# Kernel optimization log

Hardware: AMD Instinct MI355X
Metric: run time of the kernel (lower is better)

Reference implementation:

```python
import jax, jax.numpy as jnp
import numpy as np

N, E, P = 50000, 800000, 100000
IN, HID, H, L = 128, 128, 8, 3
D = HID // H


def setup_inputs() -> dict:
    key = jax.random.key(0)
    ks = jax.random.split(key, 24)
    rn = lambda k, shape, s: (jax.random.normal(k, shape, jnp.float32) * s)
    inp = {
        'x': jax.random.normal(ks[0], (N, IN), jnp.float32),
        'edge_src': jax.random.randint(ks[1], (E,), 0, N, jnp.int32),
        'edge_dst': jax.random.randint(ks[2], (E,), 0, N, jnp.int32),
        'edge_w': jax.random.uniform(ks[3], (E,), jnp.float32),
        'pos_src': jax.random.randint(ks[4], (P,), 0, N, jnp.int32),
        'pos_dst': jax.random.randint(ks[5], (P,), 0, N, jnp.int32),
        'neg_src': jax.random.randint(ks[6], (P,), 0, N, jnp.int32),
        'neg_dst': jax.random.randint(ks[7], (P,), 0, N, jnp.int32),
        # input projection
        'W_in': rn(ks[8], (IN, HID), IN ** -0.5),
        'b_in': jnp.zeros((HID,), jnp.float32),
        # per-layer HGT params (single ntype/etype -> plain matrices)
        'Wk': rn(ks[9], (L, HID, HID), HID ** -0.5),
        'Wq': rn(ks[10], (L, HID, HID), HID ** -0.5),
        'Wv': rn(ks[11], (L, HID, HID), HID ** -0.5),
        'att_w': rn(ks[12], (L, H, D, D), D ** -0.5),
        'msg_w': rn(ks[13], (L, H, D, D), D ** -0.5),
        'pri': jnp.ones((L, H), jnp.float32),
        'Wa': rn(ks[14], (L, HID, HID), HID ** -0.5),
        'skip': jnp.ones((L,), jnp.float32),
        # predictor MLP
        'W1': rn(ks[15], (HID, HID // 2), HID ** -0.5),
        'b1': jnp.zeros((HID // 2,), jnp.float32),
        'W2': rn(ks[16], (HID // 2, HID // 4), (HID // 2) ** -0.5),
        'b2': jnp.zeros((HID // 4,), jnp.float32),
        'W3': rn(ks[17], (HID // 4, 1), (HID // 4) ** -0.5),
        'b3': jnp.zeros((1,), jnp.float32),
    }
    return inp


def _hgt_forward(x, edge_src, edge_dst, edge_w, pos_src, pos_dst, neg_src, neg_dst,
                 W_in, b_in, Wk, Wq, Wv, att_w, msg_w, pri, Wa, skip,
                 W1, b1, W2, b2, W3, b3):
    n = x.shape[0]
    nheads = att_w.shape[1]
    d = att_w.shape[2]
    sqrt_d = jnp.asarray(d ** 0.5, x.dtype)
    h = jax.nn.relu(x @ W_in + b_in)
    nlayers = Wk.shape[0]
    for l in range(nlayers):
        k = (h @ Wk[l]).reshape(n, nheads, d)
        q = (h @ Wq[l]).reshape(n, nheads, d)
        v = (h @ Wv[l]).reshape(n, nheads, d)
        # relation-specific per-head transforms (etype constant -> node-level)
        kw = jnp.einsum('nhd,hde->nhe', k, att_w[l])
        mv = jnp.einsum('nhd,hde->nhe', v, msg_w[l])
        # per-edge attention logits [E, H]
        a = (kw[edge_src] * q[edge_dst]).sum(-1) * pri[l] / sqrt_d
        # edge softmax grouped by destination node
        amax = jax.ops.segment_max(a, edge_dst, num_segments=n)[edge_dst]
        ex = jnp.exp(a - amax)
        denom = jax.ops.segment_sum(ex, edge_dst, num_segments=n)[edge_dst]
        attn = ex / denom
        # weighted messages + scatter-sum  [E,H,D] -> [N,H,D]
        m = mv[edge_src] * edge_w[:, None, None] * attn[:, :, None]
        agg = jax.ops.segment_sum(m, edge_dst, num_segments=n).reshape(n, nheads * d)
        hn = agg @ Wa[l]  # linear_a (dropout is identity in eval)
        alpha = jax.nn.sigmoid(skip[l])
        h = hn * alpha + h * (1.0 - alpha)
        if l != nlayers - 1:
            h = jax.nn.relu(h)  # inter-layer relu (dropout identity)
    def predictor(z):
        z = jax.nn.leaky_relu(z @ W1 + b1, 0.2)
        z = jax.nn.leaky_relu(z @ W2 + b2, 0.2)
        return z @ W3 + b3
    h_pos = predictor(h[pos_src] * h[pos_dst])
    h_neg = predictor(h[neg_src] * h[neg_dst])
    return h_pos, h_neg, h


def reference(x, edge_src, edge_dst, edge_w, pos_src, pos_dst, neg_src, neg_dst,
              W_in, b_in, Wk, Wq, Wv, att_w, msg_w, pri, Wa, skip,
              W1, b1, W2, b2, W3, b3):
    return _hgt_forward(x, edge_src, edge_dst, edge_w, pos_src, pos_dst,
                        neg_src, neg_dst, W_in, b_in, Wk, Wq, Wv, att_w,
                        msg_w, pri, Wa, skip, W1, b1, W2, b2, W3, b3)
```

## Files before the change

### kernel.cpp

```cpp
#include <hip/hip_runtime.h>
#include <cstddef>

#define N_NODES 50000
#define N_EDGES 800000
#define N_PAIRS 100000

typedef float floatx4 __attribute__((ext_vector_type(4)));
typedef _Float16 half2v __attribute__((ext_vector_type(2)));
typedef _Float16 half4v __attribute__((ext_vector_type(4)));
typedef _Float16 half8v __attribute__((ext_vector_type(8)));

__device__ inline size_t packA(int m, int k, int K) {
  return ((size_t)((m >> 4) * (K >> 5) + (k >> 5)) << 9) +
         ((((unsigned)k >> 3) & 3) << 7) + ((m & 15) << 3) + (k & 7);
}

__device__ inline float fold_val(int l, int r, int j, const float* Wk, const float* Wq,
                                 const float* Wv, const float* att, const float* msg,
                                 const float* pri) {
  if (j >= 128 && j < 256) return Wq[(l * 128 + r) * 128 + (j - 128)];
  int jj = j & 127, hh = jj >> 4, e = jj & 15;
  const float* W = (j < 128) ? Wk : Wv;
  const float* T = (j < 128) ? att : msg;
  float s = 0.f;
#pragma unroll
  for (int d = 0; d < 16; d++)
    s += W[(l * 128 + r) * 128 + hh * 16 + d] * T[((l * 8 + hh) * 16 + d) * 16 + e];
  if (j < 128) s *= pri[l * 8 + hh] * 0.25f;
  return s;
}

__global__ void wprep_kernel(const float* __restrict__ W_in, const float* __restrict__ Wk,
                             const float* __restrict__ Wq, const float* __restrict__ Wv,
                             const float* __restrict__ att, const float* __restrict__ msg,
                             const float* __restrict__ pri, const float* __restrict__ Wa,
                             const float* __restrict__ W1, const float* __restrict__ W2,
                             _Float16* Wint, _Float16* Wcat, _Float16* Waf,
                             _Float16* W1f, _Float16* W2f) {
  int gid = blockIdx.x * 256 + threadIdx.x;
  float v;
  _Float16* dt;
  size_t o;
  if (gid < 16384) {
    int n = gid >> 7, k = gid & 127;
    v = W_in[k * 128 + n];
    dt = Wint; o = packA(n, k, 128);
  } else if (gid < 163840) {
    int t = gid - 16384;
    int l = t / 49152, u = t - l * 49152;
    int n = u >> 7, k = u & 127;
    v = fold_val(l, k, n, Wk, Wq, Wv, att, msg, pri);
    dt = Wcat + (size_t)l * 49152;
    o = packA(n, k, 128);
  } else if (gid < 212992) {
    int t = gid - 163840;
    int l = t / 16384, u = t & 16383;
    int n = u >> 7, k = u & 127;
    v = Wa[(size_t)l * 16384 + k * 128 + n];
    dt = Waf + (size_t)l * 16384;
    o = packA(n, k, 128);
  } else if (gid < 221184) {
    int u = gid - 212992;
    int n = u >> 7, k = u & 127;
    v = W1[k * 64 + n];
    dt = W1f; o = packA(n, k, 128);
  } else if (gid < 225280) {
    int u = gid - 221184;
    int n = u >> 6, k = u & 63;
    v = (n < 32) ? W2[k * 32 + n] : 0.f;
    dt = W2f; o = packA(n, k, 64);
  } else {
    return;
  }
  dt[o] = (_Float16)v;
}

__global__ void hist_kernel(const int* __restrict__ dst, int* __restrict__ deg, int E) {
  int g = blockIdx.x * blockDim.x + threadIdx.x;
  if (g < E) atomicAdd(&deg[dst[g]], 1);
}

__global__ void scanA_kernel(const int* __restrict__ deg, int* __restrict__ offs,
                             int* __restrict__ bsum, int n) {
  __shared__ int sm[256];
  int t = threadIdx.x;
  int i = blockIdx.x * 256 + t;
  int v = (i < n) ? ((deg[i] + 7) & ~7) : 0;
  sm[t] = v;
  __syncthreads();
  for (int off = 1; off < 256; off <<= 1) {
    int u = (t >= off) ? sm[t - off] : 0;
    __syncthreads();
    sm[t] += u;
    __syncthreads();
  }
  if (i < n) offs[i] = sm[t] - v;
  if (t == 255) bsum[blockIdx.x] = sm[255];
}

__global__ void scanB_kernel(const int* __restrict__ bsum, int* __restrict__ boff,
                             int* __restrict__ offs, int nb, int n) {
  __shared__ int sm[256];
  int t = threadIdx.x;
  int v = (t < nb) ? bsum[t] : 0;
  sm[t] = v;
  __syncthreads();
  for (int off = 1; off < 256; off <<= 1) {
    int u = (t >= off) ? sm[t - off] : 0;
    __syncthreads();
    sm[t] += u;
    __syncthreads();
  }
  boff[t] = sm[t] - v;
  if (t == nb - 1) offs[n] = sm[t];
}

__global__ void scanC_kernel(int* __restrict__ offs, const int* __restrict__ boff,
                             int* __restrict__ cursor, int n) {
  int i = blockIdx.x * 256 + threadIdx.x;
  if (i < n) {
    int o = offs[i] + boff[blockIdx.x];
    offs[i] = o;
    cursor[i] = o;
  }
}

__global__ void scatter_kernel(const int* __restrict__ src, const int* __restrict__ dst,
                               const float* __restrict__ w, int* __restrict__ cursor,
                               int2* __restrict__ eld, int E) {
  int g = blockIdx.x * blockDim.x + threadIdx.x;
  if (g < E) {
    int d = dst[g];
    int p = atomicAdd(&cursor[d], 1);
    eld[p] = make_int2(src[g], __float_as_int(w[g]));
  }
}

__global__ void bhist_kernel(const int* __restrict__ deg, int* __restrict__ bh, int n) {
  __shared__ int lh[256];
  int t = threadIdx.x;
  lh[t] = 0;
  __syncthreads();
  int i = blockIdx.x * 256 + t;
  if (i < n) atomicAdd(&lh[min(deg[i], 255)], 1);
  __syncthreads();
  if (lh[t]) atomicAdd(&bh[t], lh[t]);
}
__global__ void bscan_kernel(const int* __restrict__ bh, int* __restrict__ bcur) {
  __shared__ int sm[256];
  int t = threadIdx.x;
  int v = bh[255 - t];
  sm[t] = v;
  __syncthreads();
  for (int off = 1; off < 256; off <<= 1) {
    int u = (t >= off) ? sm[t - off] : 0;
    __syncthreads();
    sm[t] += u;
    __syncthreads();
  }
  bcur[255 - t] = sm[t] - v;
}
__global__ void bscatter_kernel(const int* __restrict__ deg, int* __restrict__ bcur,
                                int* __restrict__ perm, int n) {
  __shared__ int lh[256], lbase[256];
  int t = threadIdx.x;
  lh[t] = 0;
  __syncthreads();
  int i = blockIdx.x * 256 + t;
  int b = 0, local = 0;
  if (i < n) {
    b = min(deg[i], 255);
    local = atomicAdd(&lh[b], 1);
  }
  __syncthreads();
  int cnt = lh[t];
  lbase[t] = cnt ? atomicAdd(&bcur[t], cnt) : 0;
  __syncthreads();
  if (i < n) perm[lbase[b] + local] = i;
}

template <int FIRST>
__global__ __launch_bounds__(256) void fused_layer(
    const float* __restrict__ x, const _Float16* __restrict__ aggp,
    const _Float16* __restrict__ Wg1, const float* __restrict__ bias,
    const float* __restrict__ skipv, _Float16* __restrict__ hbuf,
    const _Float16* __restrict__ Wcat_l,
    _Float16* __restrict__ kwmv, _Float16* __restrict__ qbuf, int M) {
  int tid = threadIdx.x;
  int wave = tid >> 6, lane = tid & 63;
  int l16 = lane & 15, q = lane >> 4;
  int g = q, mloc = l16;
  int tile = blockIdx.x * 4 + wave;
  int m0 = tile * 16;
  bool alive = m0 < M;
  int tileC = alive ? tile : 0;

  __shared__ _Float16 htile_s[4][2048];
  __shared__ float ldsT_s[4][16 * 68];
  _Float16* htile = htile_s[wave];
  float* myT = ldsT_s[wave];

  half8v a[4];
#pragma unroll
  for (int kc = 0; kc < 4; kc++) {
    if (FIRST) {
      int row = min(m0 + l16, M - 1);
      const float* p = x + (size_t)row * 128 + kc * 32 + q * 8;
      float4 u0 = *(const float4*)p, u1 = *(const float4*)(p + 4);
      float f[8] = {u0.x, u0.y, u0.z, u0.w, u1.x, u1.y, u1.z, u1.w};
      half8v hv;
#pragma unroll
      for (int i = 0; i < 8; i++) hv[i] = (_Float16)f[i];
      a[kc] = hv;
    } else {
      a[kc] = *(const half8v*)(aggp + (size_t)tileC * 2048 + (kc << 9) + lane * 8);
    }
  }

  float alpha = 1.f, beta = 0.f;
  if (!FIRST) {
    float sv = *skipv;
    alpha = 1.f / (1.f + __expf(-sv));
    beta = 1.f - alpha;
  }

  floatx4 acc1[8];
#pragma unroll
  for (int nt = 0; nt < 8; nt++) acc1[nt] = (floatx4){0.f, 0.f, 0.f, 0.f};
#pragma unroll
  for (int kc = 0; kc < 4; kc++) {
    half8v b[8];
#pragma unroll
    for (int nt = 0; nt < 8; nt++)
      b[nt] = *(const half8v*)(Wg1 + (size_t)nt * 2048 + (kc << 9) + lane * 8);
#pragma unroll
    for (int nt = 0; nt < 8; nt++)
      acc1[nt] = __builtin_amdgcn_mfma_f32_16x16x32_f16(a[kc], b[nt], acc1[nt], 0, 0, 0);
  }

#pragma unroll
  for (int p = 0; p < 2; p++) {
    __syncthreads();
#pragma unroll
    for (int ntl = 0; ntl < 4; ntl++)
#pragma unroll
      for (int r = 0; r < 4; r++)
        myT[(q * 4 + r) * 68 + ntl * 16 + l16] = acc1[p * 4 + ntl][r];
    __syncthreads();
#pragma unroll
    for (int kc2 = 0; kc2 < 2; kc2++) {
      const float* rp = myT + mloc * 68 + kc2 * 32 + g * 8;
      floatx4 v0 = *(const floatx4*)rp;
      floatx4 v1 = *(const floatx4*)(rp + 4);
      float vals[8] = {v0[0], v0[1], v0[2], v0[3], v1[0], v1[1], v1[2], v1[3]};
      int col0 = p * 64 + kc2 * 32 + g * 8;
      size_t pbaseL = ((size_t)(tileC * 4 + (col0 >> 5)) << 9) + (size_t)lane * 8;
      if (FIRST) {
        float4 bb0 = *(const float4*)&bias[col0];
        float4 bb1 = *(const float4*)&bias[col0 + 4];
        float bbv[8] = {bb0.x, bb0.y, bb0.z, bb0.w, bb1.x, bb1.y, bb1.z, bb1.w};
#pragma unroll
        for (int j = 0; j < 8; j++) vals[j] = fmaxf(vals[j] + bbv[j], 0.f);
      } else {
        half8v hv = *(const half8v*)(hbuf + pbaseL);
#pragma unroll
        for (int j = 0; j < 8; j++)
          vals[j] = fmaxf(alpha * vals[j] + beta * (float)hv[j], 0.f);
      }
      half8v h8;
#pragma unroll
      for (int j = 0; j < 8; j++) h8[j] = (_Float16)vals[j];
      *(half8v*)(htile + (((p * 2 + kc2) << 9) + (g << 7) + (mloc << 3))) = h8;
      if (alive) *(half8v*)(hbuf + pbaseL) = h8;
    }
  }

  for (int c = 0; c < 6; c++) {
    floatx4 acc2[4];
#pragma unroll
    for (int nt = 0; nt < 4; nt++) acc2[nt] = (floatx4){0.f, 0.f, 0.f, 0.f};
#pragma unroll
    for (int kc = 0; kc < 4; kc++) {
      half8v af = *(const half8v*)(htile + ((kc << 9) + lane * 8));
      half8v b[4];
#pragma unroll
      for (int nt = 0; nt < 4; nt++)
        b[nt] = *(const half8v*)(Wcat_l + (size_t)(c * 4 + nt) * 2048 + (kc << 9) + lane * 8);
#pragma unroll
      for (int nt = 0; nt < 4; nt++)
        acc2[nt] = __builtin_amdgcn_mfma_f32_16x16x32_f16(af, b[nt], acc2[nt], 0, 0, 0);
    }
    __syncthreads();
#pragma unroll
    for (int ntl = 0; ntl < 4; ntl++)
#pragma unroll
      for (int r = 0; r < 4; r++)
        myT[(q * 4 + r) * 68 + ntl * 16 + l16] = acc2[ntl][r];
    __syncthreads();
    if (alive) {
      int row = m0 + mloc;
#pragma unroll
      for (int kc2 = 0; kc2 < 2; kc2++) {
        const float* rp = myT + mloc * 68 + kc2 * 32 + g * 8;
        floatx4 v0 = *(const floatx4*)rp;
        floatx4 v1 = *(const floatx4*)(rp + 4);
        int col0 = c * 64 + kc2 * 32 + g * 8;
        int region = col0 >> 7;
        if (region == 1) {
          half8v h8;
#pragma unroll
          for (int j = 0; j < 4; j++) {
            h8[j] = (_Float16)v0[j];
            h8[j + 4] = (_Float16)v1[j];
          }
          *(half8v*)&qbuf[(size_t)row * 128 + (col0 - 128)] = h8;
        } else {
          int cc = col0 & 127;
          size_t base = (size_t)row * 256 + (size_t)(cc >> 2) * 8 + (region == 2 ? 4 : 0);
          half4v h0, h1;
#pragma unroll
          for (int j = 0; j < 4; j++) {
            h0[j] = (_Float16)v0[j];
            h1[j] = (_Float16)v1[j];
          }
          *(half4v*)&kwmv[base] = h0;
          *(half4v*)&kwmv[base + 8] = h1;
        }
      }
    }
  }
}

__global__ __launch_bounds__(256) void gemm_last(
    const _Float16* __restrict__ aggp, const _Float16* __restrict__ Wg1,
    const float* __restrict__ skipv, const _Float16* __restrict__ hbuf,
    float* __restrict__ hfinal, _Float16* __restrict__ hrow, int M) {
  int tid = threadIdx.x;
  int wave = tid >> 6, lane = tid & 63;
  int l16 = lane & 15, q = lane >> 4;
  int g = q, mloc = l16;
  int tile = blockIdx.x * 4 + wave;
  int m0 = tile * 16;
  bool alive = m0 < M;
  int tileC = alive ? tile : 0;

  __shared__ float ldsT_s[4][16 * 68];
  float* myT = ldsT_s[wave];

  half8v a[4];
#pragma unroll
  for (int kc = 0; kc < 4; kc++)
    a[kc] = *(const half8v*)(aggp + (size_t)tileC * 2048 + (kc << 9) + lane * 8);

  float sv = *skipv;
  float alpha = 1.f / (1.f + __expf(-sv));
  float beta = 1.f - alpha;

  floatx4 acc1[8];
#pragma unroll
  for (int nt = 0; nt < 8; nt++) acc1[nt] = (floatx4){0.f, 0.f, 0.f, 0.f};
#pragma unroll
  for (int kc = 0; kc < 4; kc++) {
    half8v b[8];
#pragma unroll
    for (int nt = 0; nt < 8; nt++)
      b[nt] = *(const half8v*)(Wg1 + (size_t)nt * 2048 + (kc << 9) + lane * 8);
#pragma unroll
    for (int nt = 0; nt < 8; nt++)
      acc1[nt] = __builtin_amdgcn_mfma_f32_16x16x32_f16(a[kc], b[nt], acc1[nt], 0, 0, 0);
  }

#pragma unroll
  for (int p = 0; p < 2; p++) {
    __syncthreads();
#pragma unroll
    for (int ntl = 0; ntl < 4; ntl++)
#pragma unroll
      for (int r = 0; r < 4; r++)
        myT[(q * 4 + r) * 68 + ntl * 16 + l16] = acc1[p * 4 + ntl][r];
    __syncthreads();
    if (alive) {
      int row = m0 + mloc;
#pragma unroll
      for (int kc2 = 0; kc2 < 2; kc2++) {
        const float* rp = myT + mloc * 68 + kc2 * 32 + g * 8;
        floatx4 v0 = *(const floatx4*)rp;
        floatx4 v1 = *(const floatx4*)(rp + 4);
        float vals[8] = {v0[0], v0[1], v0[2], v0[3], v1[0], v1[1], v1[2], v1[3]};
        int col0 = p * 64 + kc2 * 32 + g * 8;
        size_t pbase = ((size_t)(tile * 4 + (col0 >> 5)) << 9) + (size_t)lane * 8;
        half8v hv = *(const half8v*)(hbuf + pbase);
#pragma unroll
        for (int j = 0; j < 8; j++) vals[j] = alpha * vals[j] + beta * (float)hv[j];
        *(float4*)&hfinal[(size_t)row * 128 + col0] =
            make_float4(vals[0], vals[1], vals[2], vals[3]);
        *(float4*)&hfinal[(size_t)row * 128 + col0 + 4] =
            make_float4(vals[4], vals[5], vals[6], vals[7]);
        half8v h8;
#pragma unroll
        for (int j = 0; j < 8; j++) h8[j] = (_Float16)vals[j];
        *(half8v*)&hrow[(size_t)row * 128 + col0] = h8;
      }
    }
  }
}

__global__ __launch_bounds__(256) void pred_fused(
    const _Float16* __restrict__ hrow,
    const int* __restrict__ ps, const int* __restrict__ pd,
    const int* __restrict__ ns, const int* __restrict__ nd,
    const _Float16* __restrict__ W1f, const float* __restrict__ b1,
    const _Float16* __restrict__ W2f, const float* __restrict__ b2,
    const float* __restrict__ W3, const float* __restrict__ b3,
    float* __restrict__ outd, int M) {
  int tid = threadIdx.x;
  int wave = tid >> 6, lane = tid & 63;
  int l16 = lane & 15, q = lane >> 4;
  int g = q, mloc = l16;
  int tile = blockIdx.x * 4 + wave;
  int m0 = tile * 16;
  bool alive = m0 < M;

  __shared__ _Float16 t1_s[4][1024];
  __shared__ float ldsT_s[4][16 * 68];
  _Float16* t1tile = t1_s[wave];
  float* myT = ldsT_s[wave];

  int gr = min(m0 + l16, M - 1);
  bool pos = gr < N_PAIRS;
  int idx = pos ? gr : gr - N_PAIRS;
  int pa = pos ? ps[idx] : ns[idx];
  int pb = pos ? pd[idx] : nd[idx];

  half8v a[4];
#pragma unroll
  for (int kc = 0; kc < 4; kc++) {
    int kbase = kc * 32 + q * 8;
    half8v ha = *(const half8v*)(hrow + (size_t)pa * 128 + kbase);
    half8v hb = *(const half8v*)(hrow + (size_t)pb * 128 + kbase);
    a[kc] = ha * hb;
  }

  floatx4 acc1[4];
#pragma unroll
  for (int nt = 0; nt < 4; nt++) acc1[nt] = (floatx4){0.f, 0.f, 0.f, 0.f};
#pragma unroll
  for (int kc = 0; kc < 4; kc++) {
    half8v b[4];
#pragma unroll
    for (int nt = 0; nt < 4; nt++)
      b[nt] = *(const half8v*)(W1f + (size_t)nt * 2048 + (kc << 9) + lane * 8);
#pragma unroll
    for (int nt = 0; nt < 4; nt++)
      acc1[nt] = __builtin_amdgcn_mfma_f32_16x16x32_f16(a[kc], b[nt], acc1[nt], 0, 0, 0);
  }

  __syncthreads();
#pragma unroll
  for (int ntl = 0; ntl < 4; ntl++)
#pragma unroll
    for (int r = 0; r < 4; r++)
      myT[(q * 4 + r) * 68 + ntl * 16 + l16] = acc1[ntl][r];
  __syncthreads();
#pragma unroll
  for (int kc2 = 0; kc2 < 2; kc2++) {
    const float* rp = myT + mloc * 68 + kc2 * 32 + g * 8;
    floatx4 v0 = *(const floatx4*)rp;
    floatx4 v1 = *(const floatx4*)(rp + 4);
    float vals[8] = {v0[0], v0[1], v0[2], v0[3], v1[0], v1[1], v1[2], v1[3]};
    int col0 = kc2 * 32 + g * 8;
    float4 bb0 = *(const float4*)&b1[col0];
    float4 bb1 = *(const float4*)&b1[col0 + 4];
    float bbv[8] = {bb0.x, bb0.y, bb0.z, bb0.w, bb1.x, bb1.y, bb1.z, bb1.w};
    half8v h8;
#pragma unroll
    for (int j = 0; j < 8; j++) {
      float v = vals[j] + bbv[j];
      v = v > 0.f ? v : 0.2f * v;
      h8[j] = (_Float16)v;
    }
    *(half8v*)(t1tile + ((kc2 << 9) + (g << 7) + (mloc << 3))) = h8;
  }

  floatx4 acc2[2];
#pragma unroll
  for (int nt = 0; nt < 2; nt++) acc2[nt] = (floatx4){0.f, 0.f, 0.f, 0.f};
#pragma unroll
  for (int kc = 0; kc < 2; kc++) {
    half8v af = *(const half8v*)(t1tile + ((kc << 9) + lane * 8));
    half8v b[2];
#pragma unroll
    for (int nt = 0; nt < 2; nt++)
      b[nt] = *(const half8v*)(W2f + (size_t)nt * 1024 + (kc << 9) + lane * 8);
#pragma unroll
    for (int nt = 0; nt < 2; nt++)
      acc2[nt] = __builtin_amdgcn_mfma_f32_16x16x32_f16(af, b[nt], acc2[nt], 0, 0, 0);
  }

  float bw[2], wv[2];
#pragma unroll
  for (int nt = 0; nt < 2; nt++) {
    int col = nt * 16 + l16;
    bw[nt] = b2[col];
    wv[nt] = W3[col];
  }
  float b3v = b3[0];
#pragma unroll
  for (int r = 0; r < 4; r++) {
    float partial = 0.f;
#pragma unroll
    for (int nt = 0; nt < 2; nt++) {
      float v = acc2[nt][r] + bw[nt];
      v = v > 0.f ? v : 0.2f * v;
      partial += v * wv[nt];
    }
    partial += __shfl_xor(partial, 1);
    partial += __shfl_xor(partial, 2);
    partial += __shfl_xor(partial, 4);
    partial += __shfl_xor(partial, 8);
    int row = m0 + q * 4 + r;
    if (l16 == 0 && alive && row < M) outd[row] = partial + b3v;
  }
}

__global__ __launch_bounds__(256) void edge_agg_kernel(
    const _Float16* __restrict__ kwmv, const _Float16* __restrict__ qbuf,
    const int* __restrict__ poffs, const int2* __restrict__ eld,
    const int* __restrict__ perm,
    _Float16* __restrict__ agg, int n) {
  int hw = (blockIdx.x * 256 + threadIdx.x) >> 5;
  int stride = gridDim.x << 3;
  int c4 = threadIdx.x & 31;
  int ch = c4 << 2;
  for (int gw = hw; gw < n; gw += stride) {
    int node = perm[gw];
    half4v qv = *(const half4v*)&qbuf[(size_t)node * 128 + ch];
    half2v q01 = {qv[0], qv[1]}, q23 = {qv[2], qv[3]};
    float m = -1e30f, s = 0.f;
    float a0 = 0.f, a1 = 0.f, a2 = 0.f, a3 = 0.f;
    int beg = poffs[node], end = poffs[node + 1];
    for (int j = beg; j < end; j += 8) {
      int2 e[8];
      half8v kvmv[8];
#pragma unroll
      for (int i = 0; i < 8; i++) {
        e[i] = eld[j + i];
        kvmv[i] = *(const half8v*)&kwmv[(size_t)max(e[i].x, 0) * 256 + (size_t)c4 * 8];
      }
      float p[8];
#pragma unroll
      for (int i = 0; i < 8; i++) {
        half2v k01 = {kvmv[i][0], kvmv[i][1]}, k23 = {kvmv[i][2], kvmv[i][3]};
        float d = __builtin_amdgcn_fdot2(
            k01, q01, __builtin_amdgcn_fdot2(k23, q23, 0.f, false), false);
        d += __shfl_xor(d, 1);
        d += __shfl_xor(d, 2);
        p[i] = (e[i].x >= 0) ? d : -1e30f;
      }
      float nm = m;
#pragma unroll
      for (int i = 0; i < 8; i++) nm = fmaxf(nm, p[i]);
      float sc = __expf(m - nm);
      float t[8];
      float ssum = 0.f;
#pragma unroll
      for (int i = 0; i < 8; i++) {
        t[i] = __expf(p[i] - nm);
        ssum += t[i];
      }
      s = s * sc + ssum;
      a0 *= sc; a1 *= sc; a2 *= sc; a3 *= sc;
#pragma unroll
      for (int i = 0; i < 8; i++) {
        float w = (e[i].x >= 0) ? __int_as_float(e[i].y) : 0.f;
        float f = t[i] * w;
        a0 += f * (float)kvmv[i][4];
        a1 += f * (float)kvmv[i][5];
        a2 += f * (float)kvmv[i][6];
        a3 += f * (float)kvmv[i][7];
      }
      m = nm;
    }
    float inv = (s > 0.f) ? 1.f / s : 0.f;
    half4v out4;
    out4[0] = (_Float16)(a0 * inv);
    out4[1] = (_Float16)(a1 * inv);
    out4[2] = (_Float16)(a2 * inv);
    out4[3] = (_Float16)(a3 * inv);
    *(half4v*)&agg[packA(node, ch, 128)] = out4;
  }
}

extern "C" void kernel_launch(void* const* d_in, const int* in_sizes, int n_in,
                              void* d_out, int out_size, void* d_ws, size_t ws_size,
                              hipStream_t stream) {
  const float* x        = (const float*)d_in[0];
  const int*   edge_src = (const int*)d_in[1];
  const int*   edge_dst = (const int*)d_in[2];
  const float* edge_w   = (const float*)d_in[3];
  const int*   pos_src  = (const int*)d_in[4];
  const int*   pos_dst  = (const int*)d_in[5];
  const int*   neg_src  = (const int*)d_in[6];
  const int*   neg_dst  = (const int*)d_in[7];
  const float* W_in     = (const float*)d_in[8];
  const float* b_in     = (const float*)d_in[9];
  const float* Wk       = (const float*)d_in[10];
  const float* Wq       = (const float*)d_in[11];
  const float* Wv       = (const float*)d_in[12];
  const float* att_w    = (const float*)d_in[13];
  const float* msg_w    = (const float*)d_in[14];
  const float* pri      = (const float*)d_in[15];
  const float* Wa       = (const float*)d_in[16];
  const float* skip     = (const float*)d_in[17];
  const float* W1       = (const float*)d_in[18];
  const float* b1       = (const float*)d_in[19];
  const float* W2       = (const float*)d_in[20];
  const float* b2       = (const float*)d_in[21];
  const float* W3       = (const float*)d_in[22];
  const float* b3       = (const float*)d_in[23];
  float* out = (float*)d_out;

  char* W = (char*)d_ws;
  _Float16*  qbuf   = (_Float16*)(W + 0);
  _Float16*  kwmv   = (_Float16*)(W + 12800000);
  _Float16*  hbuf   = (_Float16*)(W + 38400000);
  _Float16*  agg    = (_Float16*)(W + 51200000);
  _Float16*  Wint   = (_Float16*)(W + 64000000);
  _Float16*  Wcat   = (_Float16*)(W + 64032768);
  _Float16*  Waf    = (_Float16*)(W + 64327680);
  _Float16*  W1f    = (_Float16*)(W + 64425984);
  _Float16*  W2f    = (_Float16*)(W + 64442368);
  int2*      eld    = (int2*)(W + 64450560);
  int*       deg    = (int*)(W + 77250560);
  int*       poffs  = (int*)(W + 77450560);
  int*       cursor = (int*)(W + 77650576);
  int*       perm   = (int*)(W + 77850576);
  int*       bsum   = (int*)(W + 78050576);
  int*       boff   = (int*)(W + 78051600);
  int*       bh     = (int*)(W + 78052624);
  int*       bcur   = (int*)(W + 78053648);
  _Float16*  hrow   = (_Float16*)(W + 78054912);
  float* hfinal = out + 2 * N_PAIRS;

  hipMemsetAsync(deg, 0, N_NODES * sizeof(int), stream);
  hipMemsetAsync(bh, 0, 1024, stream);
  hipMemsetAsync(eld, 0xFF, 9600000, stream);

  wprep_kernel<<<880, 256, 0, stream>>>(W_in, Wk, Wq, Wv, att_w, msg_w, pri, Wa, W1, W2,
                                        Wint, Wcat, Waf, W1f, W2f);
  hist_kernel<<<(N_EDGES + 255) / 256, 256, 0, stream>>>(edge_dst, deg, N_EDGES);
  scanA_kernel<<<196, 256, 0, stream>>>(deg, poffs, bsum, N_NODES);
  scanB_kernel<<<1, 256, 0, stream>>>(bsum, boff, poffs, 196, N_NODES);
  scanC_kernel<<<196, 256, 0, stream>>>(poffs, boff, cursor, N_NODES);
  scatter_kernel<<<(N_EDGES + 255) / 256, 256, 0, stream>>>(
      edge_src, edge_dst, edge_w, cursor, eld, N_EDGES);
  bhist_kernel<<<196, 256, 0, stream>>>(deg, bh, N_NODES);
  bscan_kernel<<<1, 256, 0, stream>>>(bh, bcur);
  bscatter_kernel<<<196, 256, 0, stream>>>(deg, bcur, perm, N_NODES);

  fused_layer<1><<<782, 256, 0, stream>>>(x, nullptr, Wint, b_in, nullptr, hbuf,
                                          Wcat, kwmv, qbuf, N_NODES);
  edge_agg_kernel<<<2048, 256, 0, stream>>>(kwmv, qbuf, poffs, eld, perm, agg, N_NODES);
  fused_layer<0><<<782, 256, 0, stream>>>(nullptr, agg, Waf, nullptr, skip + 0, hbuf,
                                          Wcat + 49152, kwmv, qbuf, N_NODES);
  edge_agg_kernel<<<2048, 256, 0, stream>>>(kwmv, qbuf, poffs, eld, perm, agg, N_NODES);
  fused_layer<0><<<782, 256, 0, stream>>>(nullptr, agg, Waf + 16384, nullptr, skip + 1,
                                          hbuf, Wcat + 98304, kwmv, qbuf, N_NODES);
  edge_agg_kernel<<<2048, 256, 0, stream>>>(kwmv, qbuf, poffs, eld, perm, agg, N_NODES);
  gemm_last<<<782, 256, 0, stream>>>(agg, Waf + 32768, skip + 2, hbuf,
                                     hfinal, hrow, N_NODES);
  pred_fused<<<3125, 256, 0, stream>>>(hrow, pos_src, pos_dst, neg_src, neg_dst,
                                       W1f, b1, W2f, b2, W3, b3, out, 2 * N_PAIRS);
}
```

Measured before the change: 558.9 us.

## Software-pipeline edge gathers and drop degree-sorted node permutation

Rewrites the edge aggregation loop to double-buffer two groups of 8 edges: source indices and K/V gathers for the next 16 edges are issued before computing the current ones, so gather latency overlaps the softmax math. It removes the degree-bucket permutation (three kernels plus a memset) and processes nodes in natural order. It also adds a launch-bounds occupancy hint. The extra in-flight registers may reduce occupancy, and losing degree sorting can worsen load imbalance across half-waves.

Measured after the change: 546.0 us. -2.3%, faster.

```diff
diff --git a/kernel.cpp b/kernel.cpp
--- a/kernel.cpp
+++ b/kernel.cpp
@@ -136,49 +136,6 @@
   }
 }
 
-__global__ void bhist_kernel(const int* __restrict__ deg, int* __restrict__ bh, int n) {
-  __shared__ int lh[256];
-  int t = threadIdx.x;
-  lh[t] = 0;
-  __syncthreads();
-  int i = blockIdx.x * 256 + t;
-  if (i < n) atomicAdd(&lh[min(deg[i], 255)], 1);
-  __syncthreads();
-  if (lh[t]) atomicAdd(&bh[t], lh[t]);
-}
-__global__ void bscan_kernel(const int* __restrict__ bh, int* __restrict__ bcur) {
-  __shared__ int sm[256];
-  int t = threadIdx.x;
-  int v = bh[255 - t];
-  sm[t] = v;
-  __syncthreads();
-  for (int off = 1; off < 256; off <<= 1) {
-    int u = (t >= off) ? sm[t - off] : 0;
-    __syncthreads();
-    sm[t] += u;
-    __syncthreads();
-  }
-  bcur[255 - t] = sm[t] - v;
-}
-__global__ void bscatter_kernel(const int* __restrict__ deg, int* __restrict__ bcur,
-                                int* __restrict__ perm, int n) {
-  __shared__ int lh[256], lbase[256];
-  int t = threadIdx.x;
-  lh[t] = 0;
-  __syncthreads();
-  int i = blockIdx.x * 256 + t;
-  int b = 0, local = 0;
-  if (i < n) {
-    b = min(deg[i], 255);
-    local = atomicAdd(&lh[b], 1);
-  }
-  __syncthreads();
-  int cnt = lh[t];
-  lbase[t] = cnt ? atomicAdd(&bcur[t], cnt) : 0;
-  __syncthreads();
-  if (i < n) perm[lbase[b] + local] = i;
-}
-
 template <int FIRST>
 __global__ __launch_bounds__(256) void fused_layer(
     const float* __restrict__ x, const _Float16* __restrict__ aggp,
@@ -523,63 +480,84 @@
   }
 }
 
-__global__ __launch_bounds__(256) void edge_agg_kernel(
+#define LOAD_SRC(J, S)                                                    \
+  _Pragma("unroll") for (int i = 0; i < 8; i++) S[i] = esrc[((J) + i) * 2];
+
+#define ISSUE_G(S, G)                                                     \
+  _Pragma("unroll") for (int i = 0; i < 8; i++)                           \
+      G[i] = *(const half8v*)&kwmv[(size_t)max(S[i], 0) * 256 + lofs];
+
+#define COMPUTE(J, S, G)                                                     \
+  {                                                                          \
+    float p[8];                                                              \
+    _Pragma("unroll") for (int i = 0; i < 8; i++) {                          \
+      half2v k01 = {G[i][0], G[i][1]}, k23 = {G[i][2], G[i][3]};             \
+      float d = __builtin_amdgcn_fdot2(                                      \
+          k01, q01, __builtin_amdgcn_fdot2(k23, q23, 0.f, false), false);    \
+      d += __shfl_xor(d, 1);                                                 \
+      d += __shfl_xor(d, 2);                                                 \
+      p[i] = (S[i] >= 0) ? d : -1e30f;                                       \
+    }                                                                        \
+    float nm = m;                                                            \
+    _Pragma("unroll") for (int i = 0; i < 8; i++) nm = fmaxf(nm, p[i]);      \
+    float sc = __expf(m - nm);                                               \
+    float t[8], ssum = 0.f;                                                  \
+    _Pragma("unroll") for (int i = 0; i < 8; i++) {                          \
+      t[i] = __expf(p[i] - nm);                                              \
+      ssum += t[i];                                                          \
+    }                                                                        \
+    s = s * sc + ssum;                                                       \
+    a0 *= sc; a1 *= sc; a2 *= sc; a3 *= sc;                                  \
+    _Pragma("unroll") for (int i = 0; i < 8; i++) {                          \
+      float w = (S[i] >= 0) ? __int_as_float(esrc[((J) + i) * 2 + 1]) : 0.f; \
+      float f = t[i] * w;                                                    \
+      a0 += f * (float)G[i][4];                                              \
+      a1 += f * (float)G[i][5];                                              \
+      a2 += f * (float)G[i][6];                                              \
+      a3 += f * (float)G[i][7];                                              \
+    }                                                                        \
+    m = nm;                                                                  \
+  }
+
+__global__ __launch_bounds__(256, 3) void edge_agg_kernel(
     const _Float16* __restrict__ kwmv, const _Float16* __restrict__ qbuf,
     const int* __restrict__ poffs, const int2* __restrict__ eld,
-    const int* __restrict__ perm,
     _Float16* __restrict__ agg, int n) {
   int hw = (blockIdx.x * 256 + threadIdx.x) >> 5;
   int stride = gridDim.x << 3;
   int c4 = threadIdx.x & 31;
   int ch = c4 << 2;
-  for (int gw = hw; gw < n; gw += stride) {
-    int node = perm[gw];
+  size_t lofs = (size_t)c4 * 8;
+  const int* esrc = (const int*)eld;
+  for (int node = hw; node < n; node += stride) {
     half4v qv = *(const half4v*)&qbuf[(size_t)node * 128 + ch];
     half2v q01 = {qv[0], qv[1]}, q23 = {qv[2], qv[3]};
     float m = -1e30f, s = 0.f;
     float a0 = 0.f, a1 = 0.f, a2 = 0.f, a3 = 0.f;
     int beg = poffs[node], end = poffs[node + 1];
-    for (int j = beg; j < end; j += 8) {
-      int2 e[8];
-      half8v kvmv[8];
-#pragma unroll
-      for (int i = 0; i < 8; i++) {
-        e[i] = eld[j + i];
-        kvmv[i] = *(const half8v*)&kwmv[(size_t)max(e[i].x, 0) * 256 + (size_t)c4 * 8];
+    if (beg < end) {
+      int sA[8], sB[8], sA2[8], sB2[8];
+      half8v gA[8], gB[8];
+      LOAD_SRC(beg, sA);
+      ISSUE_G(sA, gA);
+      LOAD_SRC(beg + 8, sB);
+      ISSUE_G(sB, gB);
+      int j = beg;
+      for (; j + 16 < end; j += 16) {
+        LOAD_SRC(j + 16, sA2);
+        LOAD_SRC(j + 24, sB2);
+        COMPUTE(j, sA, gA);
+        ISSUE_G(sA2, gA);
+        COMPUTE(j + 8, sB, gB);
+        ISSUE_G(sB2, gB);
+#pragma unroll
+        for (int i = 0; i < 8; i++) {
+          sA[i] = sA2[i];
+          sB[i] = sB2[i];
+        }
       }
-      float p[8];
-#pragma unroll
-      for (int i = 0; i < 8; i++) {
-        half2v k01 = {kvmv[i][0], kvmv[i][1]}, k23 = {kvmv[i][2], kvmv[i][3]};
-        float d = __builtin_amdgcn_fdot2(
-            k01, q01, __builtin_amdgcn_fdot2(k23, q23, 0.f, false), false);
-        d += __shfl_xor(d, 1);
-        d += __shfl_xor(d, 2);
-        p[i] = (e[i].x >= 0) ? d : -1e30f;
-      }
-      float nm = m;
-#pragma unroll
-      for (int i = 0; i < 8; i++) nm = fmaxf(nm, p[i]);
-      float sc = __expf(m - nm);
-      float t[8];
-      float ssum = 0.f;
-#pragma unroll
-      for (int i = 0; i < 8; i++) {
-        t[i] = __expf(p[i] - nm);
-        ssum += t[i];
-      }
-      s = s * sc + ssum;
-      a0 *= sc; a1 *= sc; a2 *= sc; a3 *= sc;
-#pragma unroll
-      for (int i = 0; i < 8; i++) {
-        float w = (e[i].x >= 0) ? __int_as_float(e[i].y) : 0.f;
-        float f = t[i] * w;
-        a0 += f * (float)kvmv[i][4];
-        a1 += f * (float)kvmv[i][5];
-        a2 += f * (float)kvmv[i][6];
-        a3 += f * (float)kvmv[i][7];
-      }
-      m = nm;
+      COMPUTE(j, sA, gA);
+      if (j + 8 < end) COMPUTE(j + 8, sB, gB);
     }
     float inv = (s > 0.f) ? 1.f / s : 0.f;
     half4v out4;
@@ -634,16 +612,12 @@
   int*       deg    = (int*)(W + 77250560);
   int*       poffs  = (int*)(W + 77450560);
   int*       cursor = (int*)(W + 77650576);
-  int*       perm   = (int*)(W + 77850576);
   int*       bsum   = (int*)(W + 78050576);
   int*       boff   = (int*)(W + 78051600);
-  int*       bh     = (int*)(W + 78052624);
-  int*       bcur   = (int*)(W + 78053648);
   _Float16*  hrow   = (_Float16*)(W + 78054912);
   float* hfinal = out + 2 * N_PAIRS;
 
   hipMemsetAsync(deg, 0, N_NODES * sizeof(int), stream);
-  hipMemsetAsync(bh, 0, 1024, stream);
   hipMemsetAsync(eld, 0xFF, 9600000, stream);
 
   wprep_kernel<<<880, 256, 0, stream>>>(W_in, Wk, Wq, Wv, att_w, msg_w, pri, Wa, W1, W2,
@@ -654,19 +628,16 @@
   scanC_kernel<<<196, 256, 0, stream>>>(poffs, boff, cursor, N_NODES);
   scatter_kernel<<<(N_EDGES + 255) / 256, 256, 0, stream>>>(
       edge_src, edge_dst, edge_w, cursor, eld, N_EDGES);
-  bhist_kernel<<<196, 256, 0, stream>>>(deg, bh, N_NODES);
-  bscan_kernel<<<1, 256, 0, stream>>>(bh, bcur);
-  bscatter_kernel<<<196, 256, 0, stream>>>(deg, bcur, perm, N_NODES);
 
   fused_layer<1><<<782, 256, 0, stream>>>(x, nullptr, Wint, b_in, nullptr, hbuf,
                                           Wcat, kwmv, qbuf, N_NODES);
-  edge_agg_kernel<<<2048, 256, 0, stream>>>(kwmv, qbuf, poffs, eld, perm, agg, N_NODES);
+  edge_agg_kernel<<<2048, 256, 0, stream>>>(kwmv, qbuf, poffs, eld, agg, N_NODES);
   fused_layer<0><<<782, 256, 0, stream>>>(nullptr, agg, Waf, nullptr, skip + 0, hbuf,
                                           Wcat + 49152, kwmv, qbuf, N_NODES);
-  edge_agg_kernel<<<2048, 256, 0, stream>>>(kwmv, qbuf, poffs, eld, perm, agg, N_NODES);
+  edge_agg_kernel<<<2048, 256, 0, stream>>>(kwmv, qbuf, poffs, eld, agg, N_NODES);
   fused_layer<0><<<782, 256, 0, stream>>>(nullptr, agg, Waf + 16384, nullptr, skip + 1,
                                           hbuf, Wcat + 98304, kwmv, qbuf, N_NODES);
-  edge_agg_kernel<<<2048, 256, 0, stream>>>(kwmv, qbuf, poffs, eld, perm, agg, N_NODES);
+  edge_agg_kernel<<<2048, 256, 0, stream>>>(kwmv, qbuf, poffs, eld, agg, N_NODES);
   gemm_last<<<782, 256, 0, stream>>>(agg, Waf + 32768, skip + 2, hbuf,
                                      hfinal, hrow, N_NODES);
   pred_fused<<<3125, 256, 0, stream>>>(hrow, pos_src, pos_dst, neg_src, neg_dst,
```

## Software-pipeline edge gathers in attention aggregation and shrink CSR padding to 4

Applied to the files above, without the earlier changes.

The edge aggregation loop now runs as a double-buffered software pipeline. Two groups of four edges are processed in turn, and the kwmv gathers for the next group are issued before the current group is computed, with sched_barrier fences to keep that order. CSR row padding drops from multiples of 8 to multiples of 4, which cuts wasted padded edges and the size of the memset. Edge validity now comes from deg rather than a sentinel source index, and a launch_bounds occupancy hint is added. The extra in-flight registers could limit occupancy, and the tail logic adds complexity.

Result: slower. 929.3 us (+66.3%).

```diff
diff --git a/kernel.cpp b/kernel.cpp
--- a/kernel.cpp
+++ b/kernel.cpp
@@ -85,7 +85,7 @@
   __shared__ int sm[256];
   int t = threadIdx.x;
   int i = blockIdx.x * 256 + t;
-  int v = (i < n) ? ((deg[i] + 7) & ~7) : 0;
+  int v = (i < n) ? ((deg[i] + 3) & ~3) : 0;
   sm[t] = v;
   __syncthreads();
   for (int off = 1; off < 256; off <<= 1) {
@@ -523,15 +523,57 @@
   }
 }
 
-__global__ __launch_bounds__(256) void edge_agg_kernel(
+#define LOAD4(J, S)                                                       \
+  _Pragma("unroll") for (int i = 0; i < 4; i++) S[i] = esrc[((J) + i) * 2];
+
+#define ISSUE4(S, G)                                                      \
+  _Pragma("unroll") for (int i = 0; i < 4; i++)                           \
+      G[i] = *(const half8v*)&kwmv[(size_t)max(S[i], 0) * 256 + lofs];
+
+#define COMPUTE4(J, G)                                                    \
+  {                                                                       \
+    float p[4];                                                           \
+    _Pragma("unroll") for (int i = 0; i < 4; i++) {                       \
+      half2v k01 = {G[i][0], G[i][1]}, k23 = {G[i][2], G[i][3]};          \
+      float d = __builtin_amdgcn_fdot2(                                   \
+          k01, q01, __builtin_amdgcn_fdot2(k23, q23, 0.f, false), false); \
+      d += __shfl_xor(d, 1);                                              \
+      d += __shfl_xor(d, 2);                                              \
+      p[i] = ((J) + i < dend) ? d : -1e30f;                               \
+    }                                                                     \
+    float nm = m;                                                         \
+    _Pragma("unroll") for (int i = 0; i < 4; i++) nm = fmaxf(nm, p[i]);   \
+    float sc = __expf(m - nm);                                            \
+    float t[4], ssum = 0.f;                                               \
+    _Pragma("unroll") for (int i = 0; i < 4; i++) {                       \
+      t[i] = __expf(p[i] - nm);                                           \
+      ssum += t[i];                                                       \
+    }                                                                     \
+    s = s * sc + ssum;                                                    \
+    a0 *= sc; a1 *= sc; a2 *= sc; a3 *= sc;                               \
+    _Pragma("unroll") for (int i = 0; i < 4; i++) {                       \
+      float w = ((J) + i < dend)                                          \
+                    ? __int_as_float(esrc[((J) + i) * 2 + 1]) : 0.f;      \
+      float f = t[i] * w;                                                 \
+      a0 += f * (float)G[i][4];                                           \
+      a1 += f * (float)G[i][5];                                           \
+      a2 += f * (float)G[i][6];                                           \
+      a3 += f * (float)G[i][7];                                           \
+    }                                                                     \
+    m = nm;                                                               \
+  }
+
+__global__ __launch_bounds__(256, 8) void edge_agg_kernel(
     const _Float16* __restrict__ kwmv, const _Float16* __restrict__ qbuf,
     const int* __restrict__ poffs, const int2* __restrict__ eld,
-    const int* __restrict__ perm,
+    const int* __restrict__ perm, const int* __restrict__ deg,
     _Float16* __restrict__ agg, int n) {
   int hw = (blockIdx.x * 256 + threadIdx.x) >> 5;
   int stride = gridDim.x << 3;
   int c4 = threadIdx.x & 31;
   int ch = c4 << 2;
+  size_t lofs = (size_t)c4 * 8;
+  const int* esrc = (const int*)eld;
   for (int gw = hw; gw < n; gw += stride) {
     int node = perm[gw];
     half4v qv = *(const half4v*)&qbuf[(size_t)node * 128 + ch];
@@ -539,47 +581,28 @@
     float m = -1e30f, s = 0.f;
     float a0 = 0.f, a1 = 0.f, a2 = 0.f, a3 = 0.f;
     int beg = poffs[node], end = poffs[node + 1];
-    for (int j = beg; j < end; j += 8) {
-      int2 e[8];
-      half8v kvmv[8];
-#pragma unroll
-      for (int i = 0; i < 8; i++) {
-        e[i] = eld[j + i];
-        kvmv[i] = *(const half8v*)&kwmv[(size_t)max(e[i].x, 0) * 256 + (size_t)c4 * 8];
+    int dend = beg + deg[node];
+    if (beg < end) {
+      int sA[4], sB[4];
+      half8v gA[4], gB[4];
+      LOAD4(beg, sA);
+      ISSUE4(sA, gA);
+      LOAD4(beg + 4, sB);
+      ISSUE4(sB, gB);
+      __builtin_amdgcn_sched_barrier(0);
+      int j = beg;
+      for (; j + 8 < end; j += 8) {
+        LOAD4(j + 8, sA);
+        LOAD4(j + 12, sB);
+        COMPUTE4(j, gA);
+        ISSUE4(sA, gA);
+        __builtin_amdgcn_sched_barrier(0);
+        COMPUTE4(j + 4, gB);
+        ISSUE4(sB, gB);
+        __builtin_amdgcn_sched_barrier(0);
       }
-      float p[8];
-#pragma unroll
-      for (int i = 0; i < 8; i++) {
-        half2v k01 = {kvmv[i][0], kvmv[i][1]}, k23 = {kvmv[i][2], kvmv[i][3]};
-        float d = __builtin_amdgcn_fdot2(
-            k01, q01, __builtin_amdgcn_fdot2(k23, q23, 0.f, false), false);
-        d += __shfl_xor(d, 1);
-        d += __shfl_xor(d, 2);
-        p[i] = (e[i].x >= 0) ? d : -1e30f;
-      }
-      float nm = m;
-#pragma unroll
-      for (int i = 0; i < 8; i++) nm = fmaxf(nm, p[i]);
-      float sc = __expf(m - nm);
-      float t[8];
-      float ssum = 0.f;
-#pragma unroll
-      for (int i = 0; i < 8; i++) {
-        t[i] = __expf(p[i] - nm);
-        ssum += t[i];
-      }
-      s = s * sc + ssum;
-      a0 *= sc; a1 *= sc; a2 *= sc; a3 *= sc;
-#pragma unroll
-      for (int i = 0; i < 8; i++) {
-        float w = (e[i].x >= 0) ? __int_as_float(e[i].y) : 0.f;
-        float f = t[i] * w;
-        a0 += f * (float)kvmv[i][4];
-        a1 += f * (float)kvmv[i][5];
-        a2 += f * (float)kvmv[i][6];
-        a3 += f * (float)kvmv[i][7];
-      }
-      m = nm;
+      COMPUTE4(j, gA);
+      if (j + 4 < end) COMPUTE4(j + 4, gB);
     }
     float inv = (s > 0.f) ? 1.f / s : 0.f;
     half4v out4;
@@ -644,7 +667,7 @@
 
   hipMemsetAsync(deg, 0, N_NODES * sizeof(int), stream);
   hipMemsetAsync(bh, 0, 1024, stream);
-  hipMemsetAsync(eld, 0xFF, 9600000, stream);
+  hipMemsetAsync(eld, 0xFF, 8000000, stream);
 
   wprep_kernel<<<880, 256, 0, stream>>>(W_in, Wk, Wq, Wv, att_w, msg_w, pri, Wa, W1, W2,
                                         Wint, Wcat, Waf, W1f, W2f);
@@ -660,13 +683,16 @@
 
   fused_layer<1><<<782, 256, 0, stream>>>(x, nullptr, Wint, b_in, nullptr, hbuf,
                                           Wcat, kwmv, qbuf, N_NODES);
-  edge_agg_kernel<<<2048, 256, 0, stream>>>(kwmv, qbuf, poffs, eld, perm, agg, N_NODES);
+  edge_agg_kernel<<<2048, 256, 0, stream>>>(kwmv, qbuf, poffs, eld, perm, deg,
+                                            agg, N_NODES);
   fused_layer<0><<<782, 256, 0, stream>>>(nullptr, agg, Waf, nullptr, skip + 0, hbuf,
                                           Wcat + 49152, kwmv, qbuf, N_NODES);
-  edge_agg_kernel<<<2048, 256, 0, stream>>>(kwmv, qbuf, poffs, eld, perm, agg, N_NODES);
+  edge_agg_kernel<<<2048, 256, 0, stream>>>(kwmv, qbuf, poffs, eld, perm, deg,
+                                            agg, N_NODES);
   fused_layer<0><<<782, 256, 0, stream>>>(nullptr, agg, Waf + 16384, nullptr, skip + 1,
                                           hbuf, Wcat + 98304, kwmv, qbuf, N_NODES);
-  edge_agg_kernel<<<2048, 256, 0, stream>>>(kwmv, qbuf, poffs, eld, perm, agg, N_NODES);
+  edge_agg_kernel<<<2048, 256, 0, stream>>>(kwmv, qbuf, poffs, eld, perm, deg,
+                                            agg, N_NODES);
   gemm_last<<<782, 256, 0, stream>>>(agg, Waf + 32768, skip + 2, hbuf,
                                      hfinal, hrow, N_NODES);
   pred_fused<<<3125, 256, 0, stream>>>(hrow, pos_src, pos_dst, neg_src, neg_dst,
```

## Pipeline edge gathers into LDS via async global_load_lds with double buffering

Applied to the files above, without the earlier changes.

Rewrites the edge aggregation kernel so each 64-lane wave handles two degree-sorted nodes, one per half-wave. Edge metadata and source feature rows are streamed into shared memory with async global-to-LDS loads, double-buffered and paced by explicit vmcnt waits, so gathers overlap the softmax and accumulate math. Edge chunks shrink from 8 to 4, CSR padding drops from 8 to 4, and the real degree masks padded edges. This adds hand-written waitcnt and sched_barrier synchronisation and a metadata refill every 16 chunks, which is fragile to get right.

After: 561.5 us. Within noise of the previous version (+0.5%).

```diff
diff --git a/kernel.cpp b/kernel.cpp
--- a/kernel.cpp
+++ b/kernel.cpp
@@ -1,5 +1,7 @@
 #include <hip/hip_runtime.h>
 #include <cstddef>
+
+#pragma clang diagnostic ignored "-Waddress-space-conversion"
 
 #define N_NODES 50000
 #define N_EDGES 800000
@@ -85,7 +87,7 @@
   __shared__ int sm[256];
   int t = threadIdx.x;
   int i = blockIdx.x * 256 + t;
-  int v = (i < n) ? ((deg[i] + 7) & ~7) : 0;
+  int v = (i < n) ? ((deg[i] + 3) & ~3) : 0;
   sm[t] = v;
   __syncthreads();
   for (int off = 1; off < 256; off <<= 1) {
@@ -523,61 +525,148 @@
   }
 }
 
+#define WAITV4 { asm volatile("s_waitcnt vmcnt(4)" ::: "memory"); __builtin_amdgcn_sched_barrier(0); }
+#define WAITV0 { asm volatile("s_waitcnt vmcnt(0)" ::: "memory"); __builtin_amdgcn_sched_barrier(0); }
+#define LGKM0  { asm volatile("s_waitcnt lgkmcnt(0)" ::: "memory"); __builtin_amdgcn_sched_barrier(0); }
+
+#define GLD16(G, L)                                                        \
+  __builtin_amdgcn_global_load_lds(                                        \
+      (const __attribute__((address_space(1))) void*)(G),                  \
+      (__attribute__((address_space(3))) void*)(L), 16, 0, 0)
+#define GLD4(G, L)                                                         \
+  __builtin_amdgcn_global_load_lds(                                        \
+      (const __attribute__((address_space(1))) void*)(G),                  \
+      (__attribute__((address_space(3))) void*)(L), 4, 0, 0)
+
+#define META_DMA(B, BA, BB)                                                \
+  {                                                                        \
+    GLD4(em + ((size_t)(BA) + lane) * 2,     &meta_s[wave][B][0][0][0]);   \
+    GLD4(em + ((size_t)(BA) + lane) * 2 + 1, &meta_s[wave][B][0][1][0]);   \
+    GLD4(em + ((size_t)(BB) + lane) * 2,     &meta_s[wave][B][1][0][0]);   \
+    GLD4(em + ((size_t)(BB) + lane) * 2 + 1, &meta_s[wave][B][1][1][0]);   \
+  }
+
+#define GATHER_DMA(P, S)                                                   \
+  _Pragma("unroll") for (int i = 0; i < 4; i++)                            \
+      GLD16(kwmv + (size_t)max(S[i], 0) * 256 + lofs, &slab_s[wave][P][i][0][0]);
+
+#define READ_SRCS(B, WL, S)                                                \
+  _Pragma("unroll") for (int i = 0; i < 4; i++)                            \
+      S[i] = meta_s[wave][B][half][0][(WL) * 4 + i];
+
 __global__ __launch_bounds__(256) void edge_agg_kernel(
     const _Float16* __restrict__ kwmv, const _Float16* __restrict__ qbuf,
-    const int* __restrict__ poffs, const int2* __restrict__ eld,
-    const int* __restrict__ perm,
-    _Float16* __restrict__ agg, int n) {
-  int hw = (blockIdx.x * 256 + threadIdx.x) >> 5;
-  int stride = gridDim.x << 3;
-  int c4 = threadIdx.x & 31;
+    const int* __restrict__ poffs, const int* __restrict__ deg,
+    const int2* __restrict__ eld, const int* __restrict__ perm,
+    _Float16* __restrict__ agg, int npairs) {
+  __shared__ __align__(16) _Float16 slab_s[4][2][4][64][8];
+  __shared__ int meta_s[4][2][2][2][64];
+  int tid = threadIdx.x;
+  int wave = tid >> 6, lane = tid & 63;
+  int half = lane >> 5, c4 = lane & 31;
   int ch = c4 << 2;
-  for (int gw = hw; gw < n; gw += stride) {
-    int node = perm[gw];
+  size_t lofs = (size_t)c4 * 8;
+  const int* em = (const int*)eld;
+
+  {
+    half8v z = {};
+    _Float16* sl = &slab_s[0][0][0][0][0];
+    for (int i = tid; i < 2048; i += 256) *(half8v*)(sl + (size_t)i * 8) = z;
+  }
+  __syncthreads();
+
+  int ws = blockIdx.x * 4 + wave;
+  int stride = gridDim.x * 4;
+  if (ws >= npairs) return;
+
+  {
+    int nA = perm[2 * ws], nB = perm[2 * ws + 1];
+    META_DMA(0, poffs[nA], poffs[nB]);
+  }
+
+  for (int pr = ws, k = 0; pr < npairs; pr += stride, k ^= 1) {
+    int nodeA = perm[2 * pr], nodeB = perm[2 * pr + 1];
+    int begA = poffs[nodeA], begB = poffs[nodeB];
+    int node = half ? nodeB : nodeA;
+    int beg = half ? begB : begA;
+    int dg = deg[node];
+    int nc = (dg + 3) >> 2;
+    int ncU = max(nc, __shfl_xor(nc, 32));
     half4v qv = *(const half4v*)&qbuf[(size_t)node * 128 + ch];
+    (void)beg;
+    WAITV0;
     half2v q01 = {qv[0], qv[1]}, q23 = {qv[2], qv[3]};
+    int prn = pr + stride;
+    if (prn < npairs) {
+      int a2 = perm[2 * prn], b2 = perm[2 * prn + 1];
+      META_DMA(k ^ 1, poffs[a2], poffs[b2]);
+    }
     float m = -1e30f, s = 0.f;
-    float a0 = 0.f, a1 = 0.f, a2 = 0.f, a3 = 0.f;
-    int beg = poffs[node], end = poffs[node + 1];
-    for (int j = beg; j < end; j += 8) {
-      int2 e[8];
-      half8v kvmv[8];
-#pragma unroll
-      for (int i = 0; i < 8; i++) {
-        e[i] = eld[j + i];
-        kvmv[i] = *(const half8v*)&kwmv[(size_t)max(e[i].x, 0) * 256 + (size_t)c4 * 8];
+    float a0 = 0.f, a1 = 0.f, a2f = 0.f, a3 = 0.f;
+    int wbase = 0;
+    if (ncU > 0) {
+      int s4[4];
+      READ_SRCS(k, 0, s4);
+      GATHER_DMA(0, s4);
+      if (ncU > 1) {
+        READ_SRCS(k, 1, s4);
+        GATHER_DMA(1, s4);
       }
-      float p[8];
-#pragma unroll
-      for (int i = 0; i < 8; i++) {
-        half2v k01 = {kvmv[i][0], kvmv[i][1]}, k23 = {kvmv[i][2], kvmv[i][3]};
+    }
+    for (int c = 0; c < ncU; ++c) {
+      int p = c & 1;
+      if (c + 1 < ncU) { WAITV4 } else { WAITV0 }
+      half8v G[4];
+#pragma unroll
+      for (int i = 0; i < 4; i++)
+        G[i] = *(const half8v*)&slab_s[wave][p][i][lane][0];
+      int wl = c - wbase;
+      float wf[4];
+#pragma unroll
+      for (int i = 0; i < 4; i++)
+        wf[i] = __int_as_float(meta_s[wave][k][half][1][wl * 4 + i]);
+      LGKM0;
+      if (c + 2 < ncU) {
+        if (c + 2 - wbase >= 16) {
+          WAITV0;
+          META_DMA(k, begA + c * 4, begB + c * 4);
+          wbase = c;
+          WAITV0;
+        }
+        int s4[4];
+        READ_SRCS(k, c + 2 - wbase, s4);
+        GATHER_DMA(p, s4);
+      }
+      float p4[4];
+#pragma unroll
+      for (int i = 0; i < 4; i++) {
+        half2v k01 = {G[i][0], G[i][1]}, k23 = {G[i][2], G[i][3]};
         float d = __builtin_amdgcn_fdot2(
             k01, q01, __builtin_amdgcn_fdot2(k23, q23, 0.f, false), false);
         d += __shfl_xor(d, 1);
         d += __shfl_xor(d, 2);
-        p[i] = (e[i].x >= 0) ? d : -1e30f;
+        p4[i] = (c * 4 + i < dg) ? d : -1e30f;
       }
       float nm = m;
 #pragma unroll
-      for (int i = 0; i < 8; i++) nm = fmaxf(nm, p[i]);
+      for (int i = 0; i < 4; i++) nm = fmaxf(nm, p4[i]);
       float sc = __expf(m - nm);
-      float t[8];
-      float ssum = 0.f;
-#pragma unroll
-      for (int i = 0; i < 8; i++) {
-        t[i] = __expf(p[i] - nm);
-        ssum += t[i];
+      float tt[4], ssum = 0.f;
+#pragma unroll
+      for (int i = 0; i < 4; i++) {
+        tt[i] = __expf(p4[i] - nm);
+        ssum += tt[i];
       }
       s = s * sc + ssum;
-      a0 *= sc; a1 *= sc; a2 *= sc; a3 *= sc;
-#pragma unroll
-      for (int i = 0; i < 8; i++) {
-        float w = (e[i].x >= 0) ? __int_as_float(e[i].y) : 0.f;
-        float f = t[i] * w;
-        a0 += f * (float)kvmv[i][4];
-        a1 += f * (float)kvmv[i][5];
-        a2 += f * (float)kvmv[i][6];
-        a3 += f * (float)kvmv[i][7];
+      a0 *= sc; a1 *= sc; a2f *= sc; a3 *= sc;
+#pragma unroll
+      for (int i = 0; i < 4; i++) {
+        float w = (c * 4 + i < dg) ? wf[i] : 0.f;
+        float f = tt[i] * w;
+        a0 += f * (float)G[i][4];
+        a1 += f * (float)G[i][5];
+        a2f += f * (float)G[i][6];
+        a3 += f * (float)G[i][7];
       }
       m = nm;
     }
@@ -585,7 +674,7 @@
     half4v out4;
     out4[0] = (_Float16)(a0 * inv);
     out4[1] = (_Float16)(a1 * inv);
-    out4[2] = (_Float16)(a2 * inv);
+    out4[2] = (_Float16)(a2f * inv);
     out4[3] = (_Float16)(a3 * inv);
     *(half4v*)&agg[packA(node, ch, 128)] = out4;
   }
@@ -644,7 +733,7 @@
 
   hipMemsetAsync(deg, 0, N_NODES * sizeof(int), stream);
   hipMemsetAsync(bh, 0, 1024, stream);
-  hipMemsetAsync(eld, 0xFF, 9600000, stream);
+  hipMemsetAsync(eld, 0xFF, 8000000, stream);
 
   wprep_kernel<<<880, 256, 0, stream>>>(W_in, Wk, Wq, Wv, att_w, msg_w, pri, Wa, W1, W2,
                                         Wint, Wcat, Waf, W1f, W2f);
@@ -660,13 +749,16 @@
 
   fused_layer<1><<<782, 256, 0, stream>>>(x, nullptr, Wint, b_in, nullptr, hbuf,
                                           Wcat, kwmv, qbuf, N_NODES);
-  edge_agg_kernel<<<2048, 256, 0, stream>>>(kwmv, qbuf, poffs, eld, perm, agg, N_NODES);
+  edge_agg_kernel<<<1024, 256, 0, stream>>>(kwmv, qbuf, poffs, deg, eld, perm,
+                                            agg, N_NODES / 2);
   fused_layer<0><<<782, 256, 0, stream>>>(nullptr, agg, Waf, nullptr, skip + 0, hbuf,
                                           Wcat + 49152, kwmv, qbuf, N_NODES);
-  edge_agg_kernel<<<2048, 256, 0, stream>>>(kwmv, qbuf, poffs, eld, perm, agg, N_NODES);
+  edge_agg_kernel<<<1024, 256, 0, stream>>>(kwmv, qbuf, poffs, deg, eld, perm,
+                                            agg, N_NODES / 2);
   fused_layer<0><<<782, 256, 0, stream>>>(nullptr, agg, Waf + 16384, nullptr, skip + 1,
                                           hbuf, Wcat + 98304, kwmv, qbuf, N_NODES);
-  edge_agg_kernel<<<2048, 256, 0, stream>>>(kwmv, qbuf, poffs, eld, perm, agg, N_NODES);
+  edge_agg_kernel<<<1024, 256, 0, stream>>>(kwmv, qbuf, poffs, eld ? deg : deg, eld, perm,
+                                            agg, N_NODES / 2);
   gemm_last<<<782, 256, 0, stream>>>(agg, Waf + 32768, skip + 2, hbuf,
                                      hfinal, hrow, N_NODES);
   pred_fused<<<3125, 256, 0, stream>>>(hrow, pos_src, pos_dst, neg_src, neg_dst,
```
